# Kernel optimization log

Measured on AMD Instinct MI355X. Metric: run time of the kernel, lower is better.

## Reference

```python
import jax, jax.numpy as jnp
import numpy as np

E, K, D_IN, D_H, D_OUT, B = 16, 2, 256, 512, 256, 32768


def setup_inputs() -> dict:
    key = jax.random.key(0)
    ks = jax.random.split(key, 7)
    s_in = 1.0 / np.sqrt(D_IN)
    s_h = 1.0 / np.sqrt(D_H)
    return {
        "x": jax.random.normal(ks[0], (B, D_IN), jnp.float32),
        "Wg": jax.random.normal(ks[1], (D_IN, E), jnp.float32) * s_in,
        "bg": jnp.zeros((E,), jnp.float32),
        "W1": jax.random.normal(ks[2], (E, D_IN, D_H), jnp.float32) * s_in,
        "b1": jnp.zeros((E, D_H), jnp.float32),
        "W2": jax.random.normal(ks[3], (E, D_H, D_OUT), jnp.float32) * s_h,
        "b2": jnp.zeros((E, D_OUT), jnp.float32),
    }


def reference(x, Wg, bg, W1, b1, W2, b2):
    # Gating: softmax over experts, top-k, renormalize routing weights.
    probs = jax.nn.softmax(x @ Wg + bg, axis=-1)            # [B, E]
    top_vals, top_idx = jax.lax.top_k(probs, K)              # [B, K]
    w = top_vals / jnp.sum(top_vals, axis=-1, keepdims=True)  # [B, K]

    # Dense per-expert MLP over all tokens (vectorized dispatch equivalent).
    h = jax.nn.relu(jnp.einsum("bi,eih->ebh", x, W1) + b1[:, None, :])  # [E, B, Dh]
    out_e = jnp.einsum("ebh,eho->ebo", h, W2) + b2[:, None, :]          # [E, B, Do]

    # Gather each token's k assigned expert outputs and combine weighted.
    out_be = jnp.transpose(out_e, (1, 0, 2))                  # [B, E, Do]
    sel = jnp.take_along_axis(out_be, top_idx[:, :, None], axis=1)  # [B, K, Do]
    return jnp.sum(w[:, :, None] * sel, axis=1)               # [B, Do]
```

## Files before the change

### kernel.cpp

```cpp
#include <hip/hip_runtime.h>

#define E_ 16
#define DIN 256
#define DH 512
#define DOUT 256
#define BTOK 32768
#define HPAD 520

typedef _Float16 half8 __attribute__((ext_vector_type(8)));
typedef _Float16 half4v __attribute__((ext_vector_type(4)));
typedef float float4v __attribute__((ext_vector_type(4)));

#define OFF_P1      0u
#define OFF_P2      4194304u
#define OFF_XH      8388608u
#define OFF_SCR     25165824u
#define OFF_TIDX    58720256u
#define OFF_TW      58982400u
#define OFF_STOK    59244544u
#define OFF_SW      59506688u
#define OFF_CNT     59768832u
#define OFF_OFFS    59768960u
#define OFF_CUR     59769088u
#define OFF_TMAP    59769216u
#define OFF_TMC     59773504u

__global__ __launch_bounds__(256) void pack_kernel(const float* __restrict__ W1,
                                                   const float* __restrict__ W2,
                                                   _Float16* __restrict__ p1,
                                                   _Float16* __restrict__ p2,
                                                   int* __restrict__ counts) {
    int tid = threadIdx.x;
    int bid = blockIdx.x * 4 + (tid >> 6);
    int l = tid & 63;
    int quad = l >> 4, l15 = l & 15;
    if (blockIdx.x == 0 && tid < 16) counts[tid] = 0;
    if (bid < 4096) {
        int ht = bid & 31, kt = (bid >> 5) & 7, e = bid >> 8;
        half8 v;
#pragma unroll
        for (int j = 0; j < 8; ++j)
            v[j] = (_Float16)W1[(e * DIN + kt * 32 + quad * 8 + j) * DH + ht * 16 + l15];
        ((half8*)p1)[bid * 64 + l] = v;
    } else {
        int b2i = bid - 4096;
        int ot = b2i & 15, kt = (b2i >> 4) & 15, e = b2i >> 8;
        half8 v;
#pragma unroll
        for (int j = 0; j < 8; ++j)
            v[j] = (_Float16)W2[(e * DH + kt * 32 + quad * 8 + j) * DOUT + ot * 16 + l15];
        ((half8*)p2)[b2i * 64 + l] = v;
    }
}

__global__ __launch_bounds__(256) void gate_kernel(const float* __restrict__ x,
                                                   const float* __restrict__ Wg,
                                                   const float* __restrict__ bg,
                                                   _Float16* __restrict__ xh,
                                                   int* __restrict__ tidx,
                                                   float* __restrict__ tw,
                                                   int* __restrict__ counts) {
    __shared__ float WgS[DIN * E_];
    __shared__ int hcnt[16];
    int tid = threadIdx.x;
    if (tid < 16) hcnt[tid] = 0;
#pragma unroll
    for (int i = 0; i < 4; ++i)
        ((float4v*)WgS)[tid + i * 256] = ((const float4v*)Wg)[tid + i * 256];
    __syncthreads();

    int q = tid & 7, tg = tid >> 3;
    int t0 = blockIdx.x * 64 + tg * 2;

    float acc[2][16];
#pragma unroll
    for (int tt = 0; tt < 2; ++tt)
#pragma unroll
        for (int e = 0; e < 16; ++e) acc[tt][e] = 0.f;

#pragma unroll
    for (int ii = 0; ii < 8; ++ii) {
        int kb = q * 32 + ii * 4;
        float4v xv[2];
#pragma unroll
        for (int tt = 0; tt < 2; ++tt) {
            xv[tt] = *(const float4v*)&x[(t0 + tt) * DIN + kb];
            half4v hv;
#pragma unroll
            for (int j = 0; j < 4; ++j) hv[j] = (_Float16)xv[tt][j];
            *(half4v*)&xh[(t0 + tt) * DIN + kb] = hv;
        }
#pragma unroll
        for (int j = 0; j < 4; ++j) {
            const float4v* wrow = (const float4v*)&WgS[(kb + j) * 16];
            float4v w0 = wrow[0], w1 = wrow[1], w2 = wrow[2], w3 = wrow[3];
#pragma unroll
            for (int tt = 0; tt < 2; ++tt) {
                float xs = xv[tt][j];
#pragma unroll
                for (int c = 0; c < 4; ++c) {
                    acc[tt][0 + c]  += xs * w0[c];
                    acc[tt][4 + c]  += xs * w1[c];
                    acc[tt][8 + c]  += xs * w2[c];
                    acc[tt][12 + c] += xs * w3[c];
                }
            }
        }
    }
#pragma unroll
    for (int tt = 0; tt < 2; ++tt)
#pragma unroll
        for (int e = 0; e < 16; ++e) {
            acc[tt][e] += __shfl_xor(acc[tt][e], 1);
            acc[tt][e] += __shfl_xor(acc[tt][e], 2);
            acc[tt][e] += __shfl_xor(acc[tt][e], 4);
        }
    if (q == 0) {
#pragma unroll
        for (int tt = 0; tt < 2; ++tt) {
            int b = t0 + tt;
            float m1 = -3.4e38f, m2 = -3.4e38f;
            int i1 = 0, i2 = 0;
#pragma unroll
            for (int e = 0; e < 16; ++e) {
                float v = acc[tt][e] + bg[e];
                if (v > m1) { m2 = m1; i2 = i1; m1 = v; i1 = e; }
                else if (v > m2) { m2 = v; i2 = e; }
            }
            float e2 = __expf(m2 - m1);
            float w1 = 1.f / (1.f + e2);
            tidx[b * 2] = i1; tidx[b * 2 + 1] = i2;
            tw[b * 2] = w1;  tw[b * 2 + 1] = e2 * w1;
            atomicAdd(&hcnt[i1], 1);
            atomicAdd(&hcnt[i2], 1);
        }
    }
    __syncthreads();
    if (tid < 16) atomicAdd(&counts[tid], hcnt[tid]);
}

__global__ void scan_kernel(const int* __restrict__ counts, int* __restrict__ offsets,
                            int* __restrict__ cursor, int* __restrict__ tmap,
                            int* __restrict__ tmc) {
    __shared__ int s_cnt[16];
    __shared__ int s_tstart[17];
    int tid = threadIdx.x;
    if (tid == 0) {
        int run = 0, trun = 0;
        for (int e = 0; e < 16; ++e) {
            int c = counts[e];
            s_cnt[e] = c;
            offsets[e] = run; cursor[e] = run; run += c;
            s_tstart[e] = trun; trun += (c + 63) >> 6;
        }
        offsets[16] = run;
        s_tstart[16] = trun;
        tmc[0] = trun;
    }
    __syncthreads();
    if (tid < 16) {
        int nt = (s_cnt[tid] + 63) >> 6;
        int base = s_tstart[tid];
        for (int t = 0; t < nt; ++t) tmap[base + t] = (tid << 16) | t;
    }
}

__global__ __launch_bounds__(256) void scatter_kernel(const int* __restrict__ tidx,
                                                      const float* __restrict__ tw,
                                                      int* __restrict__ cursor,
                                                      int* __restrict__ stok,
                                                      float* __restrict__ sw) {
    __shared__ int lc[16];
    __shared__ int lbase[16];
    int tid = threadIdx.x;
    if (tid < 16) lc[tid] = 0;
    __syncthreads();
    int g = blockIdx.x * 256 + tid;
    int e = tidx[g];
    int rank = atomicAdd(&lc[e], 1);
    __syncthreads();
    if (tid < 16) lbase[tid] = atomicAdd(&cursor[tid], lc[tid]);
    __syncthreads();
    int pos = lbase[e] + rank;
    stok[pos] = g;
    sw[pos] = tw[g];
}

__global__ __launch_bounds__(512, 4) void mlp_kernel(const _Float16* __restrict__ xh,
                                                     const _Float16* __restrict__ p1,
                                                     const _Float16* __restrict__ p2,
                                                     const float* __restrict__ b1,
                                                     const float* __restrict__ b2,
                                                     const int* __restrict__ offsets,
                                                     const int* __restrict__ stok,
                                                     const float* __restrict__ sw,
                                                     const int* __restrict__ tmap,
                                                     const int* __restrict__ tmc,
                                                     _Float16* __restrict__ scr) {
    __shared__ _Float16 Hs[64 * HPAD];
    if ((int)blockIdx.x >= tmc[0]) return;
    const int tile = tmap[blockIdx.x];
    const int e = tile >> 16;
    const int ts = (tile & 0xffff) * 64;
    const int off = offsets[e];
    const int ne = offsets[e + 1] - off;
    const int rows = min(64, ne - ts);

    const int tid = threadIdx.x;
    const int w = tid >> 6;
    const int l = tid & 63;
    const int l15 = l & 15;
    const int quad = l >> 4;

    const _Float16* tb[4];
#pragma unroll
    for (int nt = 0; nt < 4; ++nt) {
        int r = nt * 16 + l15; if (r >= rows) r = rows - 1;
        tb[nt] = xh + (stok[off + ts + r] >> 1) * DIN + quad * 8;
    }

    const half8* p1b = (const half8*)p1;
    const half8* p2b = (const half8*)p2;

    float4v acc1[4][4];
#pragma unroll
    for (int mh = 0; mh < 4; ++mh)
#pragma unroll
        for (int nt = 0; nt < 4; ++nt) acc1[mh][nt] = (float4v){0.f, 0.f, 0.f, 0.f};

#pragma unroll
    for (int kt = 0; kt < 8; ++kt) {
        half8 bq[4];
#pragma unroll
        for (int nt = 0; nt < 4; ++nt) bq[nt] = *(const half8*)(tb[nt] + kt * 32);
#pragma unroll
        for (int mh = 0; mh < 4; ++mh) {
            half8 aw = p1b[((e * 8 + kt) * 32 + w * 4 + mh) * 64 + l];
#pragma unroll
            for (int nt = 0; nt < 4; ++nt)
                acc1[mh][nt] = __builtin_amdgcn_mfma_f32_16x16x32_f16(aw, bq[nt], acc1[mh][nt], 0, 0, 0);
        }
    }
#pragma unroll
    for (int mh = 0; mh < 4; ++mh) {
        int hb = (w * 4 + mh) * 16 + quad * 4;
        float4v b1q = *(const float4v*)&b1[e * DH + hb];
#pragma unroll
        for (int nt = 0; nt < 4; ++nt) {
            half4v hv;
#pragma unroll
            for (int r = 0; r < 4; ++r) {
                float v = acc1[mh][nt][r] + b1q[r];
                hv[r] = (_Float16)(v > 0.f ? v : 0.f);
            }
            *(half4v*)&Hs[(nt * 16 + l15) * HPAD + hb] = hv;
        }
    }
    __syncthreads();

    float4v acc2[4][2];
#pragma unroll
    for (int mt = 0; mt < 4; ++mt)
#pragma unroll
        for (int n = 0; n < 2; ++n) acc2[mt][n] = (float4v){0.f, 0.f, 0.f, 0.f};

#pragma unroll
    for (int kt2 = 0; kt2 < 16; ++kt2) {
        half8 ha[4];
#pragma unroll
        for (int mt = 0; mt < 4; ++mt)
            ha[mt] = *(const half8*)&Hs[(mt * 16 + l15) * HPAD + kt2 * 32 + quad * 8];
#pragma unroll
        for (int n = 0; n < 2; ++n) {
            half8 bw = p2b[((e * 16 + kt2) * 16 + w * 2 + n) * 64 + l];
#pragma unroll
            for (int mt = 0; mt < 4; ++mt)
                acc2[mt][n] = __builtin_amdgcn_mfma_f32_16x16x32_f16(ha[mt], bw, acc2[mt][n], 0, 0, 0);
        }
    }

    float b2v[2];
#pragma unroll
    for (int n = 0; n < 2; ++n) b2v[n] = b2[e * DOUT + (w * 2 + n) * 16 + l15];
#pragma unroll
    for (int mt = 0; mt < 4; ++mt)
#pragma unroll
        for (int r = 0; r < 4; ++r) {
            int row = mt * 16 + quad * 4 + r;
            if (row < rows) {
                int g = stok[off + ts + row];
                float wt = sw[off + ts + row];
#pragma unroll
                for (int n = 0; n < 2; ++n) {
                    int col = (w * 2 + n) * 16 + l15;
                    scr[g * DOUT + col] = (_Float16)(wt * (acc2[mt][n][r] + b2v[n]));
                }
            }
        }
}

__global__ __launch_bounds__(256) void combine_kernel(const _Float16* __restrict__ scr,
                                                      float* __restrict__ out) {
    int wv = threadIdx.x >> 6;
    int l = threadIdx.x & 63;
    int t = blockIdx.x * 4 + wv;
    half4v a = ((const half4v*)(scr + t * 2 * DOUT))[l];
    half4v b = ((const half4v*)(scr + t * 2 * DOUT + DOUT))[l];
    float4v o;
#pragma unroll
    for (int j = 0; j < 4; ++j) o[j] = (float)a[j] + (float)b[j];
    ((float4v*)(out + t * DOUT))[l] = o;
}

extern "C" void kernel_launch(void* const* d_in, const int* in_sizes, int n_in,
                              void* d_out, int out_size, void* d_ws, size_t ws_size,
                              hipStream_t stream) {
    const float* x  = (const float*)d_in[0];
    const float* Wg = (const float*)d_in[1];
    const float* bg = (const float*)d_in[2];
    const float* W1 = (const float*)d_in[3];
    const float* b1 = (const float*)d_in[4];
    const float* W2 = (const float*)d_in[5];
    const float* b2 = (const float*)d_in[6];
    float* out = (float*)d_out;

    char* ws = (char*)d_ws;
    _Float16* p1  = (_Float16*)(ws + OFF_P1);
    _Float16* p2  = (_Float16*)(ws + OFF_P2);
    _Float16* xh  = (_Float16*)(ws + OFF_XH);
    _Float16* scr = (_Float16*)(ws + OFF_SCR);
    int* tidx     = (int*)(ws + OFF_TIDX);
    float* tw     = (float*)(ws + OFF_TW);
    int* stok     = (int*)(ws + OFF_STOK);
    float* swp    = (float*)(ws + OFF_SW);
    int* counts   = (int*)(ws + OFF_CNT);
    int* offsets  = (int*)(ws + OFF_OFFS);
    int* cursor   = (int*)(ws + OFF_CUR);
    int* tmap     = (int*)(ws + OFF_TMAP);
    int* tmc      = (int*)(ws + OFF_TMC);

    pack_kernel<<<dim3(2048), dim3(256), 0, stream>>>(W1, W2, p1, p2, counts);
    gate_kernel<<<dim3(512), dim3(256), 0, stream>>>(x, Wg, bg, xh, tidx, tw, counts);
    scan_kernel<<<dim3(1), dim3(64), 0, stream>>>(counts, offsets, cursor, tmap, tmc);
    scatter_kernel<<<dim3(256), dim3(256), 0, stream>>>(tidx, tw, cursor, stok, swp);
    mlp_kernel<<<dim3(1040), dim3(512), 0, stream>>>(xh, p1, p2, b1, b2, offsets,
                                                     stok, swp, tmap, tmc, scr);
    combine_kernel<<<dim3(8192), dim3(256), 0, stream>>>(scr, out);
}
```

Baseline: 228.0 us.

## Stage tokens in swizzled LDS, split hidden dim, coalesce output, XCD-aware tile map

```diff
diff --git a/kernel.cpp b/kernel.cpp
--- a/kernel.cpp
+++ b/kernel.cpp
@@ -5,7 +5,6 @@
 #define DH 512
 #define DOUT 256
 #define BTOK 32768
-#define HPAD 520
 
 typedef _Float16 half8 __attribute__((ext_vector_type(8)));
 typedef _Float16 half4v __attribute__((ext_vector_type(4)));
@@ -23,7 +22,7 @@
 #define OFF_OFFS    59768960u
 #define OFF_CUR     59769088u
 #define OFF_TMAP    59769216u
-#define OFF_TMC     59773504u
+#define MLP_GRID    2048
 
 __global__ __launch_bounds__(256) void pack_kernel(const float* __restrict__ W1,
                                                    const float* __restrict__ W2,
@@ -140,28 +139,25 @@
 }
 
 __global__ void scan_kernel(const int* __restrict__ counts, int* __restrict__ offsets,
-                            int* __restrict__ cursor, int* __restrict__ tmap,
-                            int* __restrict__ tmc) {
-    __shared__ int s_cnt[16];
-    __shared__ int s_tstart[17];
+                            int* __restrict__ cursor, int* __restrict__ tmap) {
     int tid = threadIdx.x;
+    for (int i = tid; i < MLP_GRID; i += 64) tmap[i] = -1;
+    __syncthreads();
     if (tid == 0) {
-        int run = 0, trun = 0;
+        int run = 0;
+        int xslot[8];
+        for (int xc = 0; xc < 8; ++xc) xslot[xc] = 0;
         for (int e = 0; e < 16; ++e) {
             int c = counts[e];
-            s_cnt[e] = c;
             offsets[e] = run; cursor[e] = run; run += c;
-            s_tstart[e] = trun; trun += (c + 63) >> 6;
+            int nt = (c + 63) >> 6;
+            int xc = e & 7;
+            for (int t = 0; t < nt; ++t) {
+                int s = xslot[xc]++;
+                if (s < 256) tmap[xc + 8 * s] = (e << 16) | t;
+            }
         }
         offsets[16] = run;
-        s_tstart[16] = trun;
-        tmc[0] = trun;
-    }
-    __syncthreads();
-    if (tid < 16) {
-        int nt = (s_cnt[tid] + 63) >> 6;
-        int base = s_tstart[tid];
-        for (int t = 0; t < nt; ++t) tmap[base + t] = (tid << 16) | t;
     }
 }
 
@@ -186,6 +182,8 @@
     sw[pos] = tw[g];
 }
 
+#define XS 0
+#define HS 16384
 __global__ __launch_bounds__(512, 4) void mlp_kernel(const _Float16* __restrict__ xh,
                                                      const _Float16* __restrict__ p1,
                                                      const _Float16* __restrict__ p2,
@@ -195,11 +193,10 @@
                                                      const int* __restrict__ stok,
                                                      const float* __restrict__ sw,
                                                      const int* __restrict__ tmap,
-                                                     const int* __restrict__ tmc,
                                                      _Float16* __restrict__ scr) {
-    __shared__ _Float16 Hs[64 * HPAD];
-    if ((int)blockIdx.x >= tmc[0]) return;
+    __shared__ _Float16 S[32768];
     const int tile = tmap[blockIdx.x];
+    if (tile < 0) return;
     const int e = tile >> 16;
     const int ts = (tile & 0xffff) * 64;
     const int off = offsets[e];
@@ -212,91 +209,126 @@
     const int l15 = l & 15;
     const int quad = l >> 4;
 
-    const _Float16* tb[4];
-#pragma unroll
-    for (int nt = 0; nt < 4; ++nt) {
-        int r = nt * 16 + l15; if (r >= rows) r = rows - 1;
-        tb[nt] = xh + (stok[off + ts + r] >> 1) * DIN + quad * 8;
+#pragma unroll
+    for (int j = 0; j < 4; ++j) {
+        int tokl = w * 8 + j * 2 + (l >> 5);
+        int slot = l & 31;
+        int g = slot ^ (tokl & 7);
+        int r = tokl; if (r >= rows) r = rows - 1;
+        int tok = stok[off + ts + r] >> 1;
+        half8 v = *(const half8*)&xh[tok * DIN + g * 8];
+        *(half8*)&S[XS + tokl * 256 + slot * 8] = v;
     }
 
     const half8* p1b = (const half8*)p1;
     const half8* p2b = (const half8*)p2;
 
-    float4v acc1[4][4];
-#pragma unroll
-    for (int mh = 0; mh < 4; ++mh)
-#pragma unroll
-        for (int nt = 0; nt < 4; ++nt) acc1[mh][nt] = (float4v){0.f, 0.f, 0.f, 0.f};
-
-#pragma unroll
-    for (int kt = 0; kt < 8; ++kt) {
-        half8 bq[4];
-#pragma unroll
-        for (int nt = 0; nt < 4; ++nt) bq[nt] = *(const half8*)(tb[nt] + kt * 32);
-#pragma unroll
-        for (int mh = 0; mh < 4; ++mh) {
-            half8 aw = p1b[((e * 8 + kt) * 32 + w * 4 + mh) * 64 + l];
-#pragma unroll
-            for (int nt = 0; nt < 4; ++nt)
-                acc1[mh][nt] = __builtin_amdgcn_mfma_f32_16x16x32_f16(aw, bq[nt], acc1[mh][nt], 0, 0, 0);
-        }
-    }
-#pragma unroll
-    for (int mh = 0; mh < 4; ++mh) {
-        int hb = (w * 4 + mh) * 16 + quad * 4;
-        float4v b1q = *(const float4v*)&b1[e * DH + hb];
-#pragma unroll
-        for (int nt = 0; nt < 4; ++nt) {
-            half4v hv;
-#pragma unroll
-            for (int r = 0; r < 4; ++r) {
-                float v = acc1[mh][nt][r] + b1q[r];
-                hv[r] = (_Float16)(v > 0.f ? v : 0.f);
-            }
-            *(half4v*)&Hs[(nt * 16 + l15) * HPAD + hb] = hv;
-        }
-    }
-    __syncthreads();
-
     float4v acc2[4][2];
 #pragma unroll
     for (int mt = 0; mt < 4; ++mt)
 #pragma unroll
         for (int n = 0; n < 2; ++n) acc2[mt][n] = (float4v){0.f, 0.f, 0.f, 0.f};
 
-#pragma unroll
-    for (int kt2 = 0; kt2 < 16; ++kt2) {
-        half8 ha[4];
-#pragma unroll
-        for (int mt = 0; mt < 4; ++mt)
-            ha[mt] = *(const half8*)&Hs[(mt * 16 + l15) * HPAD + kt2 * 32 + quad * 8];
-#pragma unroll
-        for (int n = 0; n < 2; ++n) {
-            half8 bw = p2b[((e * 16 + kt2) * 16 + w * 2 + n) * 64 + l];
-#pragma unroll
-            for (int mt = 0; mt < 4; ++mt)
-                acc2[mt][n] = __builtin_amdgcn_mfma_f32_16x16x32_f16(ha[mt], bw, acc2[mt][n], 0, 0, 0);
-        }
+    __syncthreads();
+
+#pragma unroll
+    for (int half = 0; half < 2; ++half) {
+        float4v acc1[2][4];
+#pragma unroll
+        for (int mh = 0; mh < 2; ++mh)
+#pragma unroll
+            for (int nt = 0; nt < 4; ++nt) acc1[mh][nt] = (float4v){0.f, 0.f, 0.f, 0.f};
+
+#pragma unroll
+        for (int kt = 0; kt < 8; ++kt) {
+            half8 bq[4];
+#pragma unroll
+            for (int nt = 0; nt < 4; ++nt) {
+                int row = nt * 16 + l15;
+                int slot = (kt * 4 + quad) ^ (l15 & 7);
+                bq[nt] = *(const half8*)&S[XS + row * 256 + slot * 8];
+            }
+#pragma unroll
+            for (int mh = 0; mh < 2; ++mh) {
+                half8 aw = p1b[((e * 8 + kt) * 32 + half * 16 + w * 2 + mh) * 64 + l];
+#pragma unroll
+                for (int nt = 0; nt < 4; ++nt)
+                    acc1[mh][nt] = __builtin_amdgcn_mfma_f32_16x16x32_f16(aw, bq[nt], acc1[mh][nt], 0, 0, 0);
+            }
+        }
+#pragma unroll
+        for (int mh = 0; mh < 2; ++mh) {
+            int colh = (w * 2 + mh) * 16 + quad * 4;
+            float4v b1q = *(const float4v*)&b1[e * DH + half * 256 + colh];
+            int gq = colh >> 3;
+            int go = (quad & 1) * 4;
+#pragma unroll
+            for (int nt = 0; nt < 4; ++nt) {
+                int row = nt * 16 + l15;
+                int slot = gq ^ (l15 & 7);
+                half4v hv;
+#pragma unroll
+                for (int r = 0; r < 4; ++r) {
+                    float v = acc1[mh][nt][r] + b1q[r];
+                    hv[r] = (_Float16)(v > 0.f ? v : 0.f);
+                }
+                *(half4v*)&S[HS + row * 256 + slot * 8 + go] = hv;
+            }
+        }
+        __syncthreads();
+
+#pragma unroll
+        for (int kt2 = 0; kt2 < 8; ++kt2) {
+            half8 ha[4];
+#pragma unroll
+            for (int mt = 0; mt < 4; ++mt) {
+                int row = mt * 16 + l15;
+                int slot = (kt2 * 4 + quad) ^ (l15 & 7);
+                ha[mt] = *(const half8*)&S[HS + row * 256 + slot * 8];
+            }
+#pragma unroll
+            for (int n = 0; n < 2; ++n) {
+                half8 bw = p2b[((e * 16 + half * 8 + kt2) * 16 + w * 2 + n) * 64 + l];
+#pragma unroll
+                for (int mt = 0; mt < 4; ++mt)
+                    acc2[mt][n] = __builtin_amdgcn_mfma_f32_16x16x32_f16(ha[mt], bw, acc2[mt][n], 0, 0, 0);
+            }
+        }
+        __syncthreads();
     }
 
     float b2v[2];
 #pragma unroll
     for (int n = 0; n < 2; ++n) b2v[n] = b2[e * DOUT + (w * 2 + n) * 16 + l15];
 #pragma unroll
-    for (int mt = 0; mt < 4; ++mt)
+    for (int mt = 0; mt < 4; ++mt) {
 #pragma unroll
         for (int r = 0; r < 4; ++r) {
             int row = mt * 16 + quad * 4 + r;
-            if (row < rows) {
-                int g = stok[off + ts + row];
-                float wt = sw[off + ts + row];
-#pragma unroll
-                for (int n = 0; n < 2; ++n) {
-                    int col = (w * 2 + n) * 16 + l15;
-                    scr[g * DOUT + col] = (_Float16)(wt * (acc2[mt][n][r] + b2v[n]));
-                }
-            }
-        }
+            int rc = row < rows ? row : rows - 1;
+            float wt = sw[off + ts + rc];
+#pragma unroll
+            for (int n = 0; n < 2; ++n) {
+                int col = (w * 2 + n) * 16 + l15;
+                int slot = (col >> 3) ^ (row & 7);
+                S[HS + row * 256 + slot * 8 + (col & 7)] =
+                    (_Float16)(wt * (acc2[mt][n][r] + b2v[n]));
+            }
+        }
+    }
+    __syncthreads();
+#pragma unroll
+    for (int p = 0; p < 4; ++p) {
+        int idx = p * 512 + tid;
+        int tok = idx >> 5;
+        int sl = idx & 31;
+        if (tok < rows) {
+            int slot = sl ^ (tok & 7);
+            half8 v = *(const half8*)&S[HS + tok * 256 + slot * 8];
+            int g = stok[off + ts + tok];
+            *(half8*)&scr[g * DOUT + sl * 8] = v;
+        }
+    }
 }
 
 __global__ __launch_bounds__(256) void combine_kernel(const _Float16* __restrict__ scr,
@@ -337,13 +369,12 @@
     int* offsets  = (int*)(ws + OFF_OFFS);
     int* cursor   = (int*)(ws + OFF_CUR);
     int* tmap     = (int*)(ws + OFF_TMAP);
-    int* tmc      = (int*)(ws + OFF_TMC);
 
     pack_kernel<<<dim3(2048), dim3(256), 0, stream>>>(W1, W2, p1, p2, counts);
     gate_kernel<<<dim3(512), dim3(256), 0, stream>>>(x, Wg, bg, xh, tidx, tw, counts);
-    scan_kernel<<<dim3(1), dim3(64), 0, stream>>>(counts, offsets, cursor, tmap, tmc);
+    scan_kernel<<<dim3(1), dim3(64), 0, stream>>>(counts, offsets, cursor, tmap);
     scatter_kernel<<<dim3(256), dim3(256), 0, stream>>>(tidx, tw, cursor, stok, swp);
-    mlp_kernel<<<dim3(1040), dim3(512), 0, stream>>>(xh, p1, p2, b1, b2, offsets,
-                                                     stok, swp, tmap, tmc, scr);
+    mlp_kernel<<<dim3(MLP_GRID), dim3(512), 0, stream>>>(xh, p1, p2, b1, b2, offsets,
+                                                         stok, swp, tmap, scr);
     combine_kernel<<<dim3(8192), dim3(256), 0, stream>>>(scr, out);
 }
```

After: 320.1 us. 40.4% more time.
